# Optimization experiments

Hardware: AMD Instinct MI355X
Metric: run time of the kernel (lower is better)

Reference implementation:

```python
import jax, jax.numpy as jnp
import numpy as np

FEATURES = 8
MAX_LAG = 50
OMEGA, ALPHA, BETA = 0.05, 0.1, 0.85   # garch_params
NU = 4.0                               # Student-t dof (hardcoded in source)
W_ACL, W_GARCH = 10.0, 0.001           # loss_weights
LOG_2PI = float(np.log(2.0 * np.pi))


def setup_inputs() -> dict:
    key = jax.random.key(0)
    k1, k2 = jax.random.split(key)
    x_true = jax.random.normal(k1, (4096, 512, FEATURES), dtype=jnp.float32)
    dec_out = jax.random.normal(k2, (4096, 512, 2 * FEATURES), dtype=jnp.float32)
    return {"x_true": x_true, "dec_out": dec_out}


def _series(y_pred):
    # concat(seq 0 full series, last value of every other sequence) -> [T + B - 1]
    return jnp.concatenate([y_pred[0, :, 0], y_pred[1:, -1, 0]], axis=0)


def _acl_loss(y_pred):
    s = _series(y_pred)
    n = s.shape[0]
    sc = s - jnp.mean(s)
    fft_len = 2 * n
    F = jnp.fft.rfft(sc, n=fft_len)
    autocorr = jnp.fft.irfft(jnp.conj(F) * F, n=fft_len)  # real by construction
    variance = jnp.sum(jnp.square(sc))
    autocorr = autocorr[: MAX_LAG + 1] / variance
    return jnp.mean(jnp.square(autocorr[1:]))


def _garch_nll_loss(y_pred):
    s = _series(y_pred)
    r = s - jnp.mean(s)
    r2 = jnp.square(r)
    sigma0 = OMEGA / (1.0 - ALPHA - BETA)  # unconditional variance

    def step(prev_sigma_sq, cur_r2):
        new = OMEGA + ALPHA * cur_r2 + BETA * prev_sigma_sq
        return new, new

    _, cond_var = jax.lax.scan(step, sigma0, r2)
    scale = jnp.sqrt(cond_var * (NU - 2.0) / NU)
    z = r / scale
    # StudentT(df=NU, loc=0, scale).log_prob(r)
    lp = (jax.scipy.special.gammaln((NU + 1.0) / 2.0)
          - jax.scipy.special.gammaln(NU / 2.0)
          - 0.5 * jnp.log(NU * jnp.pi)
          - jnp.log(scale)
          - (NU + 1.0) / 2.0 * jnp.log1p(z * z / NU))
    return -jnp.sum(lp)


def _gaussian_nll(x_true, dec_out):
    mean = dec_out[..., :FEATURES]
    log_var = dec_out[..., FEATURES:]
    ll = -0.5 * (LOG_2PI + log_var + jnp.square(x_true - mean) * jnp.exp(-log_var))
    return -jnp.mean(jnp.sum(ll, axis=(1, 2)))


def reference(x_true, dec_out):
    y_pred = dec_out[..., :FEATURES]  # generated_x = decoder means
    recon = _gaussian_nll(x_true, dec_out)
    acl = _acl_loss(y_pred)
    garch = _garch_nll_loss(y_pred)
    return recon + W_ACL * acl + W_GARCH * garch
```

## Files before the change

kernel.cpp:

```cpp
#include <hip/hip_runtime.h>

#define NS        4607
#define NBLK1     8192
#define PX_PER_BLK 256
#define N_TOTAL   16777216.0

#define WS_SC    (NBLK1)
#define WS_VAR   (NBLK1 + NS)
#define WS_GARCH (NBLK1 + NS + 1)
#define WS_ACL   (NBLK1 + NS + 2)

__device__ __forceinline__ float wave_sum(float v) {
    for (int o = 32; o > 0; o >>= 1) v += __shfl_down(v, o);
    return v;
}

__global__ __launch_bounds__(256) void recon_kernel(
    const float* __restrict__ x, const float* __restrict__ dec,
    float* __restrict__ partials)
{
    __shared__ float ldsDec[PX_PER_BLK * 20];
    const int tid = threadIdx.x;
    const long long pixBase = (long long)blockIdx.x * PX_PER_BLK;

    const float4* dec4 = (const float4*)(dec + pixBase * 16);
#pragma unroll
    for (int s = 0; s < 4; ++s) {
        const int w   = tid + s * 256;
        const int pix = w >> 2, q = w & 3;
        float4 v = dec4[w];
        *(float4*)(&ldsDec[pix * 20 + q * 4]) = v;
    }
    __syncthreads();

    const float4* x4 = (const float4*)(x + pixBase * 8);
    float acc = 0.f;
#pragma unroll
    for (int k = 0; k < 2; ++k) {
        const int u   = tid + k * 256;
        const int pix = u >> 1, h = u & 1;
        float4 xv = x4[u];
        float4 m  = *(const float4*)(&ldsDec[pix * 20 + h * 4]);
        float4 lv = *(const float4*)(&ldsDec[pix * 20 + 8 + h * 4]);
        float d;
        d = xv.x - m.x; acc += lv.x + d * d * __expf(-lv.x);
        d = xv.y - m.y; acc += lv.y + d * d * __expf(-lv.y);
        d = xv.z - m.z; acc += lv.z + d * d * __expf(-lv.z);
        d = xv.w - m.w; acc += lv.w + d * d * __expf(-lv.w);
    }

    acc = wave_sum(acc);
    __shared__ float s4[4];
    if ((tid & 63) == 0) s4[tid >> 6] = acc;
    __syncthreads();
    if (tid == 0) partials[blockIdx.x] = s4[0] + s4[1] + s4[2] + s4[3];
}

__global__ __launch_bounds__(256) void series_kernel(
    const float* __restrict__ dec, float* __restrict__ ws)
{
    const float OMEGA = 0.05f, ALPHA = 0.1f, BETA = 0.85f;
    const int tid  = threadIdx.x;
    const int lane = tid & 63;
    const int wv   = tid >> 6;

    __shared__ float sc[NS];
    __shared__ float s4[4];
    __shared__ float chunk_e[256], chunk_p[256], chunk_in[256];

    float lsum = 0.f;
    for (int j = tid; j < NS; j += 256) {
        float v = (j < 512) ? dec[(long long)j * 16]
                            : dec[(long long)(j - 511) * 8192 + 8176];
        sc[j] = v;
        lsum += v;
    }
    lsum = wave_sum(lsum);
    __syncthreads();
    if (lane == 0) s4[wv] = lsum;
    __syncthreads();
    const float mean = (s4[0] + s4[1] + s4[2] + s4[3]) / (float)NS;

    float vsum = 0.f;
    __syncthreads();
    for (int j = tid; j < NS; j += 256) {
        float v = sc[j] - mean;
        sc[j] = v;
        ws[WS_SC + j] = v;
        vsum += v * v;
    }
    vsum = wave_sum(vsum);
    __syncthreads();
    if (lane == 0) s4[wv] = vsum;
    __syncthreads();
    const float var = s4[0] + s4[1] + s4[2] + s4[3];

    const int start = tid * 18;
    const int end   = min(start + 18, NS);
    float e = 0.f, p = 1.f;
    for (int i = start; i < end; ++i) {
        float r2 = sc[i] * sc[i];
        e = (OMEGA + ALPHA * r2) + BETA * e;
        p *= BETA;
    }
    chunk_e[tid] = e; chunk_p[tid] = p;
    __syncthreads();
    if (tid == 0) {
        float carry = 1.0f;
        for (int t = 0; t < 256; ++t) {
            chunk_in[t] = carry;
            carry = chunk_p[t] * carry + chunk_e[t];
        }
    }
    __syncthreads();
    float prev = chunk_in[tid];
    float g = 0.f;
    for (int i = start; i < end; ++i) {
        float r2 = sc[i] * sc[i];
        float cv = OMEGA + ALPHA * r2 + BETA * prev;
        prev = cv;
        g += 0.5f * logf(0.5f * cv) + 2.5f * log1pf(r2 / (2.f * cv));
    }
    g = wave_sum(g);
    __syncthreads();
    if (lane == 0) s4[wv] = g;
    __syncthreads();
    if (tid == 0) {
        ws[WS_VAR]   = var;
        ws[WS_GARCH] = s4[0] + s4[1] + s4[2] + s4[3];
    }
}

__global__ __launch_bounds__(256) void acl_kernel(float* __restrict__ ws)
{
    const int tid  = threadIdx.x;
    const int lane = tid & 63;
    const int wv   = tid >> 6;
    const int k    = blockIdx.x + 1;

    __shared__ float sc[NS];
    __shared__ float s4[4];
    for (int j = tid; j < NS; j += 256) sc[j] = ws[WS_SC + j];
    __syncthreads();

    float a = 0.f;
    for (int i = tid; i < NS - k; i += 256) a += sc[i] * sc[i + k];
    a = wave_sum(a);
    if (lane == 0) s4[wv] = a;
    __syncthreads();
    if (tid == 0) {
        float r = (s4[0] + s4[1] + s4[2] + s4[3]) / ws[WS_VAR];
        ws[WS_ACL + (k - 1)] = r * r;
    }
}

__global__ __launch_bounds__(256) void final_kernel(
    const float* __restrict__ ws, float* __restrict__ out)
{
    const int tid  = threadIdx.x;
    const int lane = tid & 63;
    const int wv   = tid >> 6;
    __shared__ double d4[4];
    __shared__ float  aclbuf[64];

    double ds = 0.0;
    for (int i = tid; i < NBLK1; i += 256) ds += (double)ws[i];
    for (int o = 32; o > 0; o >>= 1) ds += __shfl_down(ds, o);
    if (lane == 0) d4[wv] = ds;

    if (wv == 0) {
        float av = (lane < 50) ? ws[WS_ACL + lane] : 0.f;
        av = wave_sum(av);
        if (lane == 0) aclbuf[0] = av;
    }
    __syncthreads();

    if (tid == 0) {
        const double LOG_2PI = 1.8378770664093453;
        const double NEG_C = 0.9808292530117262;
        double q = d4[0] + d4[1] + d4[2] + d4[3];
        double recon = 0.5 * (q + N_TOTAL * LOG_2PI) / 4096.0;
        double acl   = (double)aclbuf[0] / 50.0;
        double garch = (double)ws[WS_GARCH] + (double)NS * NEG_C;
        out[0] = (float)(recon + 10.0 * acl + 0.001 * garch);
    }
}

extern "C" void kernel_launch(void* const* d_in, const int* in_sizes, int n_in,
                              void* d_out, int out_size, void* d_ws, size_t ws_size,
                              hipStream_t stream) {
    const float* x_true  = (const float*)d_in[0];
    const float* dec_out = (const float*)d_in[1];
    float* ws  = (float*)d_ws;
    float* out = (float*)d_out;

    recon_kernel<<<NBLK1, 256, 0, stream>>>(x_true, dec_out, ws);
    series_kernel<<<1, 256, 0, stream>>>(dec_out, ws);
    acl_kernel<<<50, 256, 0, stream>>>(ws);
    final_kernel<<<1, 256, 0, stream>>>(ws, out);
}
```

Baseline: 259.5 us.

## Fuse series extraction into recon kernel and merge GARCH/ACL into one tail kernel

```diff
diff --git a/kernel.cpp b/kernel.cpp
--- a/kernel.cpp
+++ b/kernel.cpp
@@ -2,13 +2,12 @@
 
 #define NS        4607
 #define NBLK1     8192
-#define PX_PER_BLK 256
 #define N_TOTAL   16777216.0
 
-#define WS_SC    (NBLK1)
-#define WS_VAR   (NBLK1 + NS)
-#define WS_GARCH (NBLK1 + NS + 1)
-#define WS_ACL   (NBLK1 + NS + 2)
+#define WS_PART  0
+#define WS_SRAW  8192
+#define WS_GARCH (8192 + NS)
+#define WS_ACL   (8192 + NS + 1)
 
 __device__ __forceinline__ float wave_sum(float v) {
     for (int o = 32; o > 0; o >>= 1) v += __shfl_down(v, o);
@@ -17,47 +16,57 @@
 
 __global__ __launch_bounds__(256) void recon_kernel(
     const float* __restrict__ x, const float* __restrict__ dec,
-    float* __restrict__ partials)
+    float* __restrict__ ws)
 {
-    __shared__ float ldsDec[PX_PER_BLK * 20];
+    __shared__ float ldsDec[256 * 20];
     const int tid = threadIdx.x;
-    const long long pixBase = (long long)blockIdx.x * PX_PER_BLK;
+    const long long pixBase = (long long)blockIdx.x * 256;
 
     const float4* dec4 = (const float4*)(dec + pixBase * 16);
-#pragma unroll
-    for (int s = 0; s < 4; ++s) {
-        const int w   = tid + s * 256;
-        const int pix = w >> 2, q = w & 3;
-        float4 v = dec4[w];
-        *(float4*)(&ldsDec[pix * 20 + q * 4]) = v;
+    const float4* x4   = (const float4*)(x + pixBase * 8);
+
+    float4 d0 = dec4[tid], d1 = dec4[tid + 256],
+           d2 = dec4[tid + 512], d3 = dec4[tid + 768];
+    float4 xv0 = x4[tid], xv1 = x4[tid + 256];
+
+    {
+        int w, pix, q;
+        w = tid;        pix = w >> 2; q = w & 3; *(float4*)(&ldsDec[pix*20 + q*4]) = d0;
+        w = tid + 256;  pix = w >> 2; q = w & 3; *(float4*)(&ldsDec[pix*20 + q*4]) = d1;
+        w = tid + 512;  pix = w >> 2; q = w & 3; *(float4*)(&ldsDec[pix*20 + q*4]) = d2;
+        w = tid + 768;  pix = w >> 2; q = w & 3; *(float4*)(&ldsDec[pix*20 + q*4]) = d3;
     }
     __syncthreads();
 
-    const float4* x4 = (const float4*)(x + pixBase * 8);
     float acc = 0.f;
 #pragma unroll
     for (int k = 0; k < 2; ++k) {
         const int u   = tid + k * 256;
-        const int pix = u >> 1, h = u & 1;
-        float4 xv = x4[u];
-        float4 m  = *(const float4*)(&ldsDec[pix * 20 + h * 4]);
-        float4 lv = *(const float4*)(&ldsDec[pix * 20 + 8 + h * 4]);
+        const int pl  = u >> 1, h = u & 1;
+        float4 xv = k ? xv1 : xv0;
+        float4 m  = *(const float4*)(&ldsDec[pl * 20 + h * 4]);
+        float4 lv = *(const float4*)(&ldsDec[pl * 20 + 8 + h * 4]);
         float d;
         d = xv.x - m.x; acc += lv.x + d * d * __expf(-lv.x);
         d = xv.y - m.y; acc += lv.y + d * d * __expf(-lv.y);
         d = xv.z - m.z; acc += lv.z + d * d * __expf(-lv.z);
         d = xv.w - m.w; acc += lv.w + d * d * __expf(-lv.w);
+
+        if (h == 0) {
+            const long long pix = pixBase + pl;
+            if (pix < 512)                 ws[WS_SRAW + (int)pix] = m.x;
+            else if ((pix & 511) == 511)   ws[WS_SRAW + (int)(pix >> 9) + 511] = m.x;
+        }
     }
 
     acc = wave_sum(acc);
     __shared__ float s4[4];
     if ((tid & 63) == 0) s4[tid >> 6] = acc;
     __syncthreads();
-    if (tid == 0) partials[blockIdx.x] = s4[0] + s4[1] + s4[2] + s4[3];
+    if (tid == 0) ws[WS_PART + blockIdx.x] = s4[0] + s4[1] + s4[2] + s4[3];
 }
 
-__global__ __launch_bounds__(256) void series_kernel(
-    const float* __restrict__ dec, float* __restrict__ ws)
+__global__ __launch_bounds__(256) void tail_kernel(float* __restrict__ ws)
 {
     const float OMEGA = 0.05f, ALPHA = 0.1f, BETA = 0.85f;
     const int tid  = threadIdx.x;
@@ -66,15 +75,9 @@
 
     __shared__ float sc[NS];
     __shared__ float s4[4];
-    __shared__ float chunk_e[256], chunk_p[256], chunk_in[256];
 
     float lsum = 0.f;
-    for (int j = tid; j < NS; j += 256) {
-        float v = (j < 512) ? dec[(long long)j * 16]
-                            : dec[(long long)(j - 511) * 8192 + 8176];
-        sc[j] = v;
-        lsum += v;
-    }
+    for (int j = tid; j < NS; j += 256) { float v = ws[WS_SRAW + j]; sc[j] = v; lsum += v; }
     lsum = wave_sum(lsum);
     __syncthreads();
     if (lane == 0) s4[wv] = lsum;
@@ -83,74 +86,58 @@
 
     float vsum = 0.f;
     __syncthreads();
-    for (int j = tid; j < NS; j += 256) {
-        float v = sc[j] - mean;
-        sc[j] = v;
-        ws[WS_SC + j] = v;
-        vsum += v * v;
-    }
+    for (int j = tid; j < NS; j += 256) { float v = sc[j] - mean; sc[j] = v; vsum += v * v; }
     vsum = wave_sum(vsum);
     __syncthreads();
     if (lane == 0) s4[wv] = vsum;
     __syncthreads();
     const float var = s4[0] + s4[1] + s4[2] + s4[3];
 
-    const int start = tid * 18;
-    const int end   = min(start + 18, NS);
-    float e = 0.f, p = 1.f;
-    for (int i = start; i < end; ++i) {
-        float r2 = sc[i] * sc[i];
-        e = (OMEGA + ALPHA * r2) + BETA * e;
-        p *= BETA;
-    }
-    chunk_e[tid] = e; chunk_p[tid] = p;
-    __syncthreads();
-    if (tid == 0) {
-        float carry = 1.0f;
-        for (int t = 0; t < 256; ++t) {
-            chunk_in[t] = carry;
-            carry = chunk_p[t] * carry + chunk_e[t];
+    if (blockIdx.x == 0) {
+        const int start = tid * 18;
+        const int end   = min(start + 18, NS);
+        float e = 0.f, p = 1.f;
+        for (int i = start; i < end; ++i) {
+            float r2 = sc[i] * sc[i];
+            e = (OMEGA + ALPHA * r2) + BETA * e;
+            p *= BETA;
         }
-    }
-    __syncthreads();
-    float prev = chunk_in[tid];
-    float g = 0.f;
-    for (int i = start; i < end; ++i) {
-        float r2 = sc[i] * sc[i];
-        float cv = OMEGA + ALPHA * r2 + BETA * prev;
-        prev = cv;
-        g += 0.5f * logf(0.5f * cv) + 2.5f * log1pf(r2 / (2.f * cv));
-    }
-    g = wave_sum(g);
-    __syncthreads();
-    if (lane == 0) s4[wv] = g;
-    __syncthreads();
-    if (tid == 0) {
-        ws[WS_VAR]   = var;
-        ws[WS_GARCH] = s4[0] + s4[1] + s4[2] + s4[3];
-    }
-}
-
-__global__ __launch_bounds__(256) void acl_kernel(float* __restrict__ ws)
-{
-    const int tid  = threadIdx.x;
-    const int lane = tid & 63;
-    const int wv   = tid >> 6;
-    const int k    = blockIdx.x + 1;
-
-    __shared__ float sc[NS];
-    __shared__ float s4[4];
-    for (int j = tid; j < NS; j += 256) sc[j] = ws[WS_SC + j];
-    __syncthreads();
-
-    float a = 0.f;
-    for (int i = tid; i < NS - k; i += 256) a += sc[i] * sc[i + k];
-    a = wave_sum(a);
-    if (lane == 0) s4[wv] = a;
-    __syncthreads();
-    if (tid == 0) {
-        float r = (s4[0] + s4[1] + s4[2] + s4[3]) / ws[WS_VAR];
-        ws[WS_ACL + (k - 1)] = r * r;
+        for (int o = 1; o < 64; o <<= 1) {
+            float pe = __shfl_up(e, o), pp = __shfl_up(p, o);
+            if (lane >= o) { e = e + p * pe; p = p * pp; }
+        }
+        __shared__ float wE[4], wP[4];
+        if (lane == 63) { wE[wv] = e; wP[wv] = p; }
+        __syncthreads();
+        float cE = 0.f, cP = 1.f;
+        for (int t = 0; t < wv; ++t) { cE = wE[t] + wP[t] * cE; cP = wP[t] * cP; }
+        float eE = __shfl_up(e, 1), eP = __shfl_up(p, 1);
+        if (lane == 0) { eE = 0.f; eP = 1.f; }
+        float prev = (eE + eP * cE) + (eP * cP) * 1.0f;
+        float g = 0.f;
+        for (int i = start; i < end; ++i) {
+            float r2 = sc[i] * sc[i];
+            float cv = OMEGA + ALPHA * r2 + BETA * prev;
+            prev = cv;
+            g += 0.5f * logf(0.5f * cv) + 2.5f * log1pf(r2 / (2.f * cv));
+        }
+        g = wave_sum(g);
+        __syncthreads();
+        if (lane == 0) s4[wv] = g;
+        __syncthreads();
+        if (tid == 0) ws[WS_GARCH] = s4[0] + s4[1] + s4[2] + s4[3];
+    } else {
+        const int k = blockIdx.x;
+        float a = 0.f;
+        for (int i = tid; i < NS - k; i += 256) a += sc[i] * sc[i + k];
+        a = wave_sum(a);
+        __syncthreads();
+        if (lane == 0) s4[wv] = a;
+        __syncthreads();
+        if (tid == 0) {
+            float r = (s4[0] + s4[1] + s4[2] + s4[3]) / var;
+            ws[WS_ACL + (k - 1)] = r * r;
+        }
     }
 }
 
@@ -161,10 +148,10 @@
     const int lane = tid & 63;
     const int wv   = tid >> 6;
     __shared__ double d4[4];
-    __shared__ float  aclbuf[64];
+    __shared__ float  aclbuf[1];
 
     double ds = 0.0;
-    for (int i = tid; i < NBLK1; i += 256) ds += (double)ws[i];
+    for (int i = tid; i < NBLK1; i += 256) ds += (double)ws[WS_PART + i];
     for (int o = 32; o > 0; o >>= 1) ds += __shfl_down(ds, o);
     if (lane == 0) d4[wv] = ds;
 
@@ -195,7 +182,6 @@
     float* out = (float*)d_out;
 
     recon_kernel<<<NBLK1, 256, 0, stream>>>(x_true, dec_out, ws);
-    series_kernel<<<1, 256, 0, stream>>>(dec_out, ws);
-    acl_kernel<<<50, 256, 0, stream>>>(ws);
+    tail_kernel<<<51, 256, 0, stream>>>(ws);
     final_kernel<<<1, 256, 0, stream>>>(ws, out);
 }
```

Measured after the change: 252.3 us. -2.8%, faster.
